# Performance work log

Measured on AMD Instinct MI355X. Metric: run time of the kernel, lower is better.

## Reference

```python
import math
import jax, jax.numpy as jnp
import numpy as np

LENGTHS = [1024, 768, 512, 1024, 256, 896, 640, 512]  # ragged seq lens, sum = 5632
NEG = -10000.0  # mask fill value used by the torch module


def setup_inputs() -> dict:
    key = jax.random.key(0)
    k1, k2 = jax.random.split(key)
    total = int(sum(LENGTHS))  # 5632 packed tokens
    H, HKV, D = 16, 4, 64      # GQA: 16 query heads, 4 kv heads
    q = jax.random.normal(k1, (total, H, D), dtype=jnp.float32)
    kv = jax.random.normal(k2, (total, 2, HKV, D), dtype=jnp.float32)
    cu_seqlens = jnp.asarray(np.concatenate([[0], np.cumsum(LENGTHS)]), dtype=jnp.int32)
    return {"q": q, "kv": kv, "cu_seqlens": cu_seqlens, "max_seqlen": 1024}


def _varlen_attention(q, kv, cu_seqlens, max_seqlen):
    # GQA repeat: '... hkv d -> ... (hkv g) d' == repeat each kv head g times
    g = q.shape[1] // kv.shape[2]
    kv = jnp.repeat(kv, g, axis=2)
    k, v = kv[:, 0], kv[:, 1]            # [total, H, D]

    starts = cu_seqlens[:-1]
    lens = cu_seqlens[1:] - starts       # [B]
    S = max_seqlen
    pos = jnp.arange(S)
    gather_idx = starts[:, None] + pos[None, :]          # [B, S]
    key_mask = pos[None, :] < lens[:, None]              # [B, S] True = valid
    gather_idx = jnp.where(key_mask, gather_idx, 0)

    m = key_mask[:, :, None, None]
    # pad ragged tokens into dense [B, S, H, D] buffers (zeros where invalid)
    qp = jnp.where(m, q[gather_idx], 0.0)
    kp = jnp.where(m, k[gather_idx], 0.0)
    vp = jnp.where(m, v[gather_idx], 0.0)

    scale = 1.0 / math.sqrt(q.shape[-1])
    scores = jnp.einsum('bthd,bshd->bhts', qp, kp * scale)   # [B, H, S, S]
    # key padding mask: 0 on valid keys, -10000 on padded keys
    scores = scores + jnp.where(key_mask, 0.0, NEG)[:, None, None, :]
    # causal mask: triu(-10000, 1)
    scores = scores + jnp.triu(jnp.full((S, S), NEG, dtype=scores.dtype), 1)

    attn = jax.nn.softmax(scores, axis=-1)
    out_padded = jnp.einsum('bhts,bshd->bthd', attn, vp)     # [B, S, H, D]

    # unpad back to packed [total, H, D]
    tok = jnp.arange(q.shape[0])
    b = jnp.searchsorted(cu_seqlens, tok, side='right') - 1  # batch id per token
    s = tok - starts[b]                                      # position within seq
    return out_padded[b, s]


def reference(q, kv, cu_seqlens, max_seqlen):
    return _varlen_attention(q, kv, cu_seqlens, max_seqlen)
```

## Files before the change

### kernel.cpp

```cpp
#include <hip/hip_runtime.h>


#define H    16
#define HKV  4
#define D    64
#define BM   16
#define BN   64
#define KSTR 72
#define NEGF (-1e30f)

using bf8 = __attribute__((ext_vector_type(8))) short;
using s4v = __attribute__((ext_vector_type(4))) short;
using f4v = __attribute__((ext_vector_type(4))) float;

__device__ inline short f2b(float x) {
    union { float f; unsigned u; } v; v.f = x;
    return (short)((v.u + 0x8000u) >> 16);
}

__global__ __launch_bounds__(256, 4)
void attn3(const float* __restrict__ q, const float* __restrict__ kv,
           const int* __restrict__ cu, float* __restrict__ out,
           int nb, int total)
{
    __shared__ __attribute__((aligned(16))) short Ks[BN * KSTR];
    __shared__ __attribute__((aligned(16))) short Vt[D * KSTR];
    __shared__ __attribute__((aligned(16))) short Ps[4][BM * KSTR];

    const int kvh = blockIdx.y;

    int bid = blockIdx.x, b = -1, start = 0, len = 0, q0 = 0, acc = 0;
    for (int i = 0; i < nb; ++i) {
        int s0 = cu[i], l = cu[i + 1] - s0, nt = (l + BM - 1) / BM;
        if (bid < acc + nt) { b = i; start = s0; len = l; q0 = (nt - 1 - (bid - acc)) * BM; break; }
        acc += nt;
    }
    if (b < 0) return;

    const int t = threadIdx.x, w = t >> 6, lane = t & 63;
    const int qd = lane >> 4, c = lane & 15;
    const int h = kvh * 4 + w;
    const int rows = min(BM, len - q0), kend = q0 + rows;
    const float SC = 0.125f * 1.44269504f;

    bf8 qf0, qf1;
    {
        int qr = min(c, rows - 1);
        const float* qp = q + (size_t)(start + q0 + qr) * (H * D) + h * D + qd * 8;
        float4 a0 = *(const float4*)qp;
        float4 a1 = *(const float4*)(qp + 4);
        float4 a2 = *(const float4*)(qp + 32);
        float4 a3 = *(const float4*)(qp + 36);
        qf0[0] = f2b(a0.x * SC); qf0[1] = f2b(a0.y * SC); qf0[2] = f2b(a0.z * SC); qf0[3] = f2b(a0.w * SC);
        qf0[4] = f2b(a1.x * SC); qf0[5] = f2b(a1.y * SC); qf0[6] = f2b(a1.z * SC); qf0[7] = f2b(a1.w * SC);
        qf1[0] = f2b(a2.x * SC); qf1[1] = f2b(a2.y * SC); qf1[2] = f2b(a2.z * SC); qf1[3] = f2b(a2.w * SC);
        qf1[4] = f2b(a3.x * SC); qf1[5] = f2b(a3.y * SC); qf1[6] = f2b(a3.z * SC); qf1[7] = f2b(a3.w * SC);
    }

    const int kd4 = t & 15, kr0 = t >> 4;
    const int vd  = t & 63, vg0 = t >> 6;

    float4 kreg[4];
    float  vreg[4][4];

    auto prefetch = [&](int kt0) {
        #pragma unroll
        for (int i = 0; i < 4; ++i) {
            int tok = min(start + kt0 + kr0 + 16 * i, total - 1);
            kreg[i] = *(const float4*)&kv[(size_t)tok * (2 * HKV * D) + kvh * D + kd4 * 4];
        }
        #pragma unroll
        for (int i = 0; i < 4; ++i) {
            int kg = vg0 + 4 * i;
            #pragma unroll
            for (int m = 0; m < 4; ++m) {
                int tok = min(start + kt0 + kg * 4 + m, total - 1);
                vreg[i][m] = kv[(size_t)tok * (2 * HKV * D) + (HKV + kvh) * D + vd];
            }
        }
    };

    float m_i = NEGF, l_i = 0.f;
    f4v o0 = {0,0,0,0}, o1 = {0,0,0,0}, o2 = {0,0,0,0}, o3 = {0,0,0,0};
    short* Psw = &Ps[w][0];

    prefetch(0);

    for (int kt0 = 0; kt0 < kend; kt0 += BN) {
        __syncthreads();
        #pragma unroll
        for (int i = 0; i < 4; ++i) {
            s4v p; p[0] = f2b(kreg[i].x); p[1] = f2b(kreg[i].y);
                   p[2] = f2b(kreg[i].z); p[3] = f2b(kreg[i].w);
            *(s4v*)&Ks[(kr0 + 16 * i) * KSTR + kd4 * 4] = p;
        }
        #pragma unroll
        for (int i = 0; i < 4; ++i) {
            int kg = vg0 + 4 * i;
            s4v p; p[0] = f2b(vreg[i][0]); p[1] = f2b(vreg[i][1]);
                   p[2] = f2b(vreg[i][2]); p[3] = f2b(vreg[i][3]);
            *(s4v*)&Vt[vd * KSTR + kg * 4] = p;
        }
        __syncthreads();

        if (kt0 + BN < kend) prefetch(kt0 + BN);

        f4v s0 = {0,0,0,0}, s1 = {0,0,0,0}, s2 = {0,0,0,0}, s3 = {0,0,0,0};
        {
            bf8 ka, kb;
            ka = *(const bf8*)&Ks[(c     ) * KSTR + qd * 8];
            kb = *(const bf8*)&Ks[(c     ) * KSTR + 32 + qd * 8];
            s0 = __builtin_amdgcn_mfma_f32_16x16x32_bf16(ka, qf0, s0, 0, 0, 0);
            s0 = __builtin_amdgcn_mfma_f32_16x16x32_bf16(kb, qf1, s0, 0, 0, 0);
            ka = *(const bf8*)&Ks[(16 + c) * KSTR + qd * 8];
            kb = *(const bf8*)&Ks[(16 + c) * KSTR + 32 + qd * 8];
            s1 = __builtin_amdgcn_mfma_f32_16x16x32_bf16(ka, qf0, s1, 0, 0, 0);
            s1 = __builtin_amdgcn_mfma_f32_16x16x32_bf16(kb, qf1, s1, 0, 0, 0);
            ka = *(const bf8*)&Ks[(32 + c) * KSTR + qd * 8];
            kb = *(const bf8*)&Ks[(32 + c) * KSTR + 32 + qd * 8];
            s2 = __builtin_amdgcn_mfma_f32_16x16x32_bf16(ka, qf0, s2, 0, 0, 0);
            s2 = __builtin_amdgcn_mfma_f32_16x16x32_bf16(kb, qf1, s2, 0, 0, 0);
            ka = *(const bf8*)&Ks[(48 + c) * KSTR + qd * 8];
            kb = *(const bf8*)&Ks[(48 + c) * KSTR + 32 + qd * 8];
            s3 = __builtin_amdgcn_mfma_f32_16x16x32_bf16(ka, qf0, s3, 0, 0, 0);
            s3 = __builtin_amdgcn_mfma_f32_16x16x32_bf16(kb, qf1, s3, 0, 0, 0);
        }

        const int limit = q0 + c - kt0;
        float sc[16];
        #pragma unroll
        for (int r = 0; r < 4; ++r) {
            sc[r]      = (      4 * qd + r <= limit) ? s0[r] : NEGF;
            sc[4 + r]  = (16 +  4 * qd + r <= limit) ? s1[r] : NEGF;
            sc[8 + r]  = (32 +  4 * qd + r <= limit) ? s2[r] : NEGF;
            sc[12 + r] = (48 +  4 * qd + r <= limit) ? s3[r] : NEGF;
        }
        float mt = sc[0];
        #pragma unroll
        for (int i = 1; i < 16; ++i) mt = fmaxf(mt, sc[i]);
        mt = fmaxf(mt, __shfl_xor(mt, 16, 64));
        mt = fmaxf(mt, __shfl_xor(mt, 32, 64));
        const float m_new = fmaxf(m_i, mt);
        const float alpha = exp2f(m_i - m_new);
        float ps = 0.f;
        #pragma unroll
        for (int i = 0; i < 16; ++i) { sc[i] = exp2f(sc[i] - m_new); ps += sc[i]; }
        ps += __shfl_xor(ps, 16, 64);
        ps += __shfl_xor(ps, 32, 64);
        l_i = l_i * alpha + ps;
        m_i = m_new;
        o0 *= alpha; o1 *= alpha; o2 *= alpha; o3 *= alpha;

        #pragma unroll
        for (int j = 0; j < 4; ++j) {
            s4v p; p[0] = f2b(sc[4 * j]);     p[1] = f2b(sc[4 * j + 1]);
                   p[2] = f2b(sc[4 * j + 2]); p[3] = f2b(sc[4 * j + 3]);
            *(s4v*)&Psw[c * KSTR + 16 * j + 4 * qd] = p;
        }
        bf8 p0 = *(const bf8*)&Psw[c * KSTR + qd * 8];
        bf8 p1 = *(const bf8*)&Psw[c * KSTR + 32 + qd * 8];

        o0 = __builtin_amdgcn_mfma_f32_16x16x32_bf16(*(const bf8*)&Vt[(c     ) * KSTR + qd * 8],      p0, o0, 0, 0, 0);
        o0 = __builtin_amdgcn_mfma_f32_16x16x32_bf16(*(const bf8*)&Vt[(c     ) * KSTR + 32 + qd * 8], p1, o0, 0, 0, 0);
        o1 = __builtin_amdgcn_mfma_f32_16x16x32_bf16(*(const bf8*)&Vt[(16 + c) * KSTR + qd * 8],      p0, o1, 0, 0, 0);
        o1 = __builtin_amdgcn_mfma_f32_16x16x32_bf16(*(const bf8*)&Vt[(16 + c) * KSTR + 32 + qd * 8], p1, o1, 0, 0, 0);
        o2 = __builtin_amdgcn_mfma_f32_16x16x32_bf16(*(const bf8*)&Vt[(32 + c) * KSTR + qd * 8],      p0, o2, 0, 0, 0);
        o2 = __builtin_amdgcn_mfma_f32_16x16x32_bf16(*(const bf8*)&Vt[(32 + c) * KSTR + 32 + qd * 8], p1, o2, 0, 0, 0);
        o3 = __builtin_amdgcn_mfma_f32_16x16x32_bf16(*(const bf8*)&Vt[(48 + c) * KSTR + qd * 8],      p0, o3, 0, 0, 0);
        o3 = __builtin_amdgcn_mfma_f32_16x16x32_bf16(*(const bf8*)&Vt[(48 + c) * KSTR + 32 + qd * 8], p1, o3, 0, 0, 0);
    }

    if (c < rows) {
        const float inv = 1.f / l_i;
        float* op = out + (size_t)(start + q0 + c) * (H * D) + h * D + 4 * qd;
        *(float4*)(op)      = make_float4(o0[0] * inv, o0[1] * inv, o0[2] * inv, o0[3] * inv);
        *(float4*)(op + 16) = make_float4(o1[0] * inv, o1[1] * inv, o1[2] * inv, o1[3] * inv);
        *(float4*)(op + 32) = make_float4(o2[0] * inv, o2[1] * inv, o2[2] * inv, o2[3] * inv);
        *(float4*)(op + 48) = make_float4(o3[0] * inv, o3[1] * inv, o3[2] * inv, o3[3] * inv);
    }
}

extern "C" void kernel_launch(void* const* d_in, const int* in_sizes, int n_in,
                              void* d_out, int out_size, void* d_ws, size_t ws_size,
                              hipStream_t stream) {
    const float* q  = (const float*)d_in[0];
    const float* kv = (const float*)d_in[1];
    const int*   cu = (const int*)d_in[2];
    float* out = (float*)d_out;

    const int total = in_sizes[0] / (H * D);
    const int nb    = in_sizes[2] - 1;
    const int tile_ub = total / BM + nb;

    dim3 grid(tile_ub, HKV);
    attn3<<<grid, 256, 0, stream>>>(q, kv, cu, out, nb, total);
}
```

Measured before the change: 129.6 us.

## Split KV loop across two warp groups with LDS merge of softmax partials

```diff
diff --git a/kernel.cpp b/kernel.cpp
--- a/kernel.cpp
+++ b/kernel.cpp
@@ -10,22 +10,27 @@
 #define NEGF (-1e30f)
 
 using bf8 = __attribute__((ext_vector_type(8))) short;
-using s4v = __attribute__((ext_vector_type(4))) short;
 using f4v = __attribute__((ext_vector_type(4))) float;
-
-__device__ inline short f2b(float x) {
-    union { float f; unsigned u; } v; v.f = x;
-    return (short)((v.u + 0x8000u) >> 16);
+typedef unsigned int u32;
+
+union bf8u { bf8 v; u32 w[4]; };
+
+__device__ inline u32 pk(float a, float b) {
+    union { float f; u32 u; } x, y; x.f = a; y.f = b;
+    return __builtin_amdgcn_perm(y.u + 0x8000u, x.u + 0x8000u, 0x07060302u);
 }
 
-__global__ __launch_bounds__(256, 4)
-void attn3(const float* __restrict__ q, const float* __restrict__ kv,
+#define MFMA(A, B, C) __builtin_amdgcn_mfma_f32_16x16x32_bf16(A, B, C, 0, 0, 0)
+
+__global__ __launch_bounds__(512, 4)
+void attn4(const float* __restrict__ q, const float* __restrict__ kv,
            const int* __restrict__ cu, float* __restrict__ out,
            int nb, int total)
 {
-    __shared__ __attribute__((aligned(16))) short Ks[BN * KSTR];
-    __shared__ __attribute__((aligned(16))) short Vt[D * KSTR];
-    __shared__ __attribute__((aligned(16))) short Ps[4][BM * KSTR];
+    __shared__ __attribute__((aligned(16))) short Ks[2][BN * KSTR];
+    __shared__ __attribute__((aligned(16))) short Vt[2][D * KSTR];
+    __shared__ __attribute__((aligned(16))) short Ps[8][BM * KSTR];
+    __shared__ float ML[4][BM][2];
 
     const int kvh = blockIdx.y;
 
@@ -38,12 +43,15 @@
     if (b < 0) return;
 
     const int t = threadIdx.x, w = t >> 6, lane = t & 63;
+    const int head = w & 3, g = w >> 2, u = t & 255;
     const int qd = lane >> 4, c = lane & 15;
-    const int h = kvh * 4 + w;
+    const int h = kvh * 4 + head;
     const int rows = min(BM, len - q0), kend = q0 + rows;
+    const int niter = (kend + BN - 1) >> 6;
+    const int trips = (niter + 1) >> 1;
     const float SC = 0.125f * 1.44269504f;
 
-    bf8 qf0, qf1;
+    bf8u qf0, qf1;
     {
         int qr = min(c, rows - 1);
         const float* qp = q + (size_t)(start + q0 + qr) * (H * D) + h * D + qd * 8;
@@ -51,90 +59,96 @@
         float4 a1 = *(const float4*)(qp + 4);
         float4 a2 = *(const float4*)(qp + 32);
         float4 a3 = *(const float4*)(qp + 36);
-        qf0[0] = f2b(a0.x * SC); qf0[1] = f2b(a0.y * SC); qf0[2] = f2b(a0.z * SC); qf0[3] = f2b(a0.w * SC);
-        qf0[4] = f2b(a1.x * SC); qf0[5] = f2b(a1.y * SC); qf0[6] = f2b(a1.z * SC); qf0[7] = f2b(a1.w * SC);
-        qf1[0] = f2b(a2.x * SC); qf1[1] = f2b(a2.y * SC); qf1[2] = f2b(a2.z * SC); qf1[3] = f2b(a2.w * SC);
-        qf1[4] = f2b(a3.x * SC); qf1[5] = f2b(a3.y * SC); qf1[6] = f2b(a3.z * SC); qf1[7] = f2b(a3.w * SC);
-    }
-
-    const int kd4 = t & 15, kr0 = t >> 4;
-    const int vd  = t & 63, vg0 = t >> 6;
-
-    float4 kreg[4];
-    float  vreg[4][4];
+        qf0.w[0] = pk(a0.x * SC, a0.y * SC); qf0.w[1] = pk(a0.z * SC, a0.w * SC);
+        qf0.w[2] = pk(a1.x * SC, a1.y * SC); qf0.w[3] = pk(a1.z * SC, a1.w * SC);
+        qf1.w[0] = pk(a2.x * SC, a2.y * SC); qf1.w[1] = pk(a2.z * SC, a2.w * SC);
+        qf1.w[2] = pk(a3.x * SC, a3.y * SC); qf1.w[3] = pk(a3.z * SC, a3.w * SC);
+    }
+
+    const int kd4 = u & 15, kr = u >> 4;
+    const int vkp = u & 15, vd4 = u >> 4;
+    const float* kbase = kv + kvh * D;
+    const float* vbase = kv + (HKV + kvh) * D;
+    float4 kreg[4], vreg[2][2];
 
     auto prefetch = [&](int kt0) {
         #pragma unroll
         for (int i = 0; i < 4; ++i) {
-            int tok = min(start + kt0 + kr0 + 16 * i, total - 1);
-            kreg[i] = *(const float4*)&kv[(size_t)tok * (2 * HKV * D) + kvh * D + kd4 * 4];
-        }
-        #pragma unroll
-        for (int i = 0; i < 4; ++i) {
-            int kg = vg0 + 4 * i;
-            #pragma unroll
-            for (int m = 0; m < 4; ++m) {
-                int tok = min(start + kt0 + kg * 4 + m, total - 1);
-                vreg[i][m] = kv[(size_t)tok * (2 * HKV * D) + (HKV + kvh) * D + vd];
-            }
+            int tok = min(start + kt0 + kr + 16 * i, total - 1);
+            kreg[i] = *(const float4*)(kbase + (size_t)tok * 512 + kd4 * 4);
+        }
+        #pragma unroll
+        for (int p = 0; p < 2; ++p) {
+            int k0 = start + kt0 + 2 * vkp + 32 * p;
+            int t0 = min(k0, total - 1), t1 = min(k0 + 1, total - 1);
+            vreg[p][0] = *(const float4*)(vbase + (size_t)t0 * 512 + vd4 * 4);
+            vreg[p][1] = *(const float4*)(vbase + (size_t)t1 * 512 + vd4 * 4);
         }
     };
 
     float m_i = NEGF, l_i = 0.f;
     f4v o0 = {0,0,0,0}, o1 = {0,0,0,0}, o2 = {0,0,0,0}, o3 = {0,0,0,0};
     short* Psw = &Ps[w][0];
-
-    prefetch(0);
-
-    for (int kt0 = 0; kt0 < kend; kt0 += BN) {
+    short* Kg  = &Ks[g][0];
+    short* Vg  = &Vt[g][0];
+
+    prefetch(g * BN);
+
+    for (int tp = 0; tp < trips; ++tp) {
+        const int it = 2 * tp + g, kt0 = it * BN;
+        const bool valid = it < niter;
         __syncthreads();
-        #pragma unroll
-        for (int i = 0; i < 4; ++i) {
-            s4v p; p[0] = f2b(kreg[i].x); p[1] = f2b(kreg[i].y);
-                   p[2] = f2b(kreg[i].z); p[3] = f2b(kreg[i].w);
-            *(s4v*)&Ks[(kr0 + 16 * i) * KSTR + kd4 * 4] = p;
-        }
-        #pragma unroll
-        for (int i = 0; i < 4; ++i) {
-            int kg = vg0 + 4 * i;
-            s4v p; p[0] = f2b(vreg[i][0]); p[1] = f2b(vreg[i][1]);
-                   p[2] = f2b(vreg[i][2]); p[3] = f2b(vreg[i][3]);
-            *(s4v*)&Vt[vd * KSTR + kg * 4] = p;
+        if (valid) {
+            #pragma unroll
+            for (int i = 0; i < 4; ++i) {
+                u32 lo = pk(kreg[i].x, kreg[i].y), hi = pk(kreg[i].z, kreg[i].w);
+                *(uint2*)&Kg[(kr + 16 * i) * KSTR + kd4 * 4] = make_uint2(lo, hi);
+            }
+            #pragma unroll
+            for (int p = 0; p < 2; ++p) {
+                const float* va = &vreg[p][0].x;
+                const float* vb = &vreg[p][1].x;
+                #pragma unroll
+                for (int j = 0; j < 4; ++j)
+                    *(u32*)&Vg[(4 * vd4 + j) * KSTR + 2 * vkp + 32 * p] = pk(va[j], vb[j]);
+            }
         }
         __syncthreads();
 
-        if (kt0 + BN < kend) prefetch(kt0 + BN);
+        if (2 * tp + 2 + g < niter) prefetch((2 * tp + 2 + g) * BN);
+        if (!valid) continue;
 
         f4v s0 = {0,0,0,0}, s1 = {0,0,0,0}, s2 = {0,0,0,0}, s3 = {0,0,0,0};
         {
             bf8 ka, kb;
-            ka = *(const bf8*)&Ks[(c     ) * KSTR + qd * 8];
-            kb = *(const bf8*)&Ks[(c     ) * KSTR + 32 + qd * 8];
-            s0 = __builtin_amdgcn_mfma_f32_16x16x32_bf16(ka, qf0, s0, 0, 0, 0);
-            s0 = __builtin_amdgcn_mfma_f32_16x16x32_bf16(kb, qf1, s0, 0, 0, 0);
-            ka = *(const bf8*)&Ks[(16 + c) * KSTR + qd * 8];
-            kb = *(const bf8*)&Ks[(16 + c) * KSTR + 32 + qd * 8];
-            s1 = __builtin_amdgcn_mfma_f32_16x16x32_bf16(ka, qf0, s1, 0, 0, 0);
-            s1 = __builtin_amdgcn_mfma_f32_16x16x32_bf16(kb, qf1, s1, 0, 0, 0);
-            ka = *(const bf8*)&Ks[(32 + c) * KSTR + qd * 8];
-            kb = *(const bf8*)&Ks[(32 + c) * KSTR + 32 + qd * 8];
-            s2 = __builtin_amdgcn_mfma_f32_16x16x32_bf16(ka, qf0, s2, 0, 0, 0);
-            s2 = __builtin_amdgcn_mfma_f32_16x16x32_bf16(kb, qf1, s2, 0, 0, 0);
-            ka = *(const bf8*)&Ks[(48 + c) * KSTR + qd * 8];
-            kb = *(const bf8*)&Ks[(48 + c) * KSTR + 32 + qd * 8];
-            s3 = __builtin_amdgcn_mfma_f32_16x16x32_bf16(ka, qf0, s3, 0, 0, 0);
-            s3 = __builtin_amdgcn_mfma_f32_16x16x32_bf16(kb, qf1, s3, 0, 0, 0);
-        }
-
-        const int limit = q0 + c - kt0;
+            ka = *(const bf8*)&Kg[(c     ) * KSTR + qd * 8];
+            kb = *(const bf8*)&Kg[(c     ) * KSTR + 32 + qd * 8];
+            s0 = MFMA(ka, qf0.v, s0); s0 = MFMA(kb, qf1.v, s0);
+            ka = *(const bf8*)&Kg[(16 + c) * KSTR + qd * 8];
+            kb = *(const bf8*)&Kg[(16 + c) * KSTR + 32 + qd * 8];
+            s1 = MFMA(ka, qf0.v, s1); s1 = MFMA(kb, qf1.v, s1);
+            ka = *(const bf8*)&Kg[(32 + c) * KSTR + qd * 8];
+            kb = *(const bf8*)&Kg[(32 + c) * KSTR + 32 + qd * 8];
+            s2 = MFMA(ka, qf0.v, s2); s2 = MFMA(kb, qf1.v, s2);
+            ka = *(const bf8*)&Kg[(48 + c) * KSTR + qd * 8];
+            kb = *(const bf8*)&Kg[(48 + c) * KSTR + 32 + qd * 8];
+            s3 = MFMA(ka, qf0.v, s3); s3 = MFMA(kb, qf1.v, s3);
+        }
+
         float sc[16];
         #pragma unroll
         for (int r = 0; r < 4; ++r) {
-            sc[r]      = (      4 * qd + r <= limit) ? s0[r] : NEGF;
-            sc[4 + r]  = (16 +  4 * qd + r <= limit) ? s1[r] : NEGF;
-            sc[8 + r]  = (32 +  4 * qd + r <= limit) ? s2[r] : NEGF;
-            sc[12 + r] = (48 +  4 * qd + r <= limit) ? s3[r] : NEGF;
-        }
+            sc[r] = s0[r]; sc[4 + r] = s1[r]; sc[8 + r] = s2[r]; sc[12 + r] = s3[r];
+        }
+        if (kt0 + 63 > q0) {
+            const int limit = q0 + c - kt0;
+            #pragma unroll
+            for (int j = 0; j < 4; ++j)
+                #pragma unroll
+                for (int r = 0; r < 4; ++r)
+                    if (16 * j + 4 * qd + r > limit) sc[4 * j + r] = NEGF;
+        }
+
         float mt = sc[0];
         #pragma unroll
         for (int i = 1; i < 16; ++i) mt = fmaxf(mt, sc[i]);
@@ -153,30 +167,49 @@
 
         #pragma unroll
         for (int j = 0; j < 4; ++j) {
-            s4v p; p[0] = f2b(sc[4 * j]);     p[1] = f2b(sc[4 * j + 1]);
-                   p[2] = f2b(sc[4 * j + 2]); p[3] = f2b(sc[4 * j + 3]);
-            *(s4v*)&Psw[c * KSTR + 16 * j + 4 * qd] = p;
+            u32 lo = pk(sc[4 * j], sc[4 * j + 1]), hi = pk(sc[4 * j + 2], sc[4 * j + 3]);
+            *(uint2*)&Psw[c * KSTR + 16 * j + 4 * qd] = make_uint2(lo, hi);
         }
         bf8 p0 = *(const bf8*)&Psw[c * KSTR + qd * 8];
         bf8 p1 = *(const bf8*)&Psw[c * KSTR + 32 + qd * 8];
 
-        o0 = __builtin_amdgcn_mfma_f32_16x16x32_bf16(*(const bf8*)&Vt[(c     ) * KSTR + qd * 8],      p0, o0, 0, 0, 0);
-        o0 = __builtin_amdgcn_mfma_f32_16x16x32_bf16(*(const bf8*)&Vt[(c     ) * KSTR + 32 + qd * 8], p1, o0, 0, 0, 0);
-        o1 = __builtin_amdgcn_mfma_f32_16x16x32_bf16(*(const bf8*)&Vt[(16 + c) * KSTR + qd * 8],      p0, o1, 0, 0, 0);
-        o1 = __builtin_amdgcn_mfma_f32_16x16x32_bf16(*(const bf8*)&Vt[(16 + c) * KSTR + 32 + qd * 8], p1, o1, 0, 0, 0);
-        o2 = __builtin_amdgcn_mfma_f32_16x16x32_bf16(*(const bf8*)&Vt[(32 + c) * KSTR + qd * 8],      p0, o2, 0, 0, 0);
-        o2 = __builtin_amdgcn_mfma_f32_16x16x32_bf16(*(const bf8*)&Vt[(32 + c) * KSTR + 32 + qd * 8], p1, o2, 0, 0, 0);
-        o3 = __builtin_amdgcn_mfma_f32_16x16x32_bf16(*(const bf8*)&Vt[(48 + c) * KSTR + qd * 8],      p0, o3, 0, 0, 0);
-        o3 = __builtin_amdgcn_mfma_f32_16x16x32_bf16(*(const bf8*)&Vt[(48 + c) * KSTR + 32 + qd * 8], p1, o3, 0, 0, 0);
-    }
-
-    if (c < rows) {
-        const float inv = 1.f / l_i;
+        o0 = MFMA(*(const bf8*)&Vg[(c     ) * KSTR + qd * 8],      p0, o0);
+        o0 = MFMA(*(const bf8*)&Vg[(c     ) * KSTR + 32 + qd * 8], p1, o0);
+        o1 = MFMA(*(const bf8*)&Vg[(16 + c) * KSTR + qd * 8],      p0, o1);
+        o1 = MFMA(*(const bf8*)&Vg[(16 + c) * KSTR + 32 + qd * 8], p1, o1);
+        o2 = MFMA(*(const bf8*)&Vg[(32 + c) * KSTR + qd * 8],      p0, o2);
+        o2 = MFMA(*(const bf8*)&Vg[(32 + c) * KSTR + 32 + qd * 8], p1, o2);
+        o3 = MFMA(*(const bf8*)&Vg[(48 + c) * KSTR + qd * 8],      p0, o3);
+        o3 = MFMA(*(const bf8*)&Vg[(48 + c) * KSTR + 32 + qd * 8], p1, o3);
+    }
+
+    float* CB = (float*)&Ks[0][0];
+    __syncthreads();
+    if (g == 1) {
+        float* cb = CB + (((head << 6) + lane) << 4);
+        *(f4v*)(cb)      = o0; *(f4v*)(cb + 4)  = o1;
+        *(f4v*)(cb + 8)  = o2; *(f4v*)(cb + 12) = o3;
+        if (qd == 0) { ML[head][c][0] = m_i; ML[head][c][1] = l_i; }
+    }
+    __syncthreads();
+    if (g == 0 && c < rows) {
+        const float* cb = CB + (((head << 6) + lane) << 4);
+        f4v r0 = *(const f4v*)(cb),     r1 = *(const f4v*)(cb + 4);
+        f4v r2 = *(const f4v*)(cb + 8), r3 = *(const f4v*)(cb + 12);
+        const float m2 = ML[head][c][0], l2 = ML[head][c][1];
+        const float M  = fmaxf(m_i, m2);
+        float a1 = exp2f(m_i - M), a2 = exp2f(m2 - M);
+        const float inv = 1.f / (l_i * a1 + l2 * a2);
+        a1 *= inv; a2 *= inv;
         float* op = out + (size_t)(start + q0 + c) * (H * D) + h * D + 4 * qd;
-        *(float4*)(op)      = make_float4(o0[0] * inv, o0[1] * inv, o0[2] * inv, o0[3] * inv);
-        *(float4*)(op + 16) = make_float4(o1[0] * inv, o1[1] * inv, o1[2] * inv, o1[3] * inv);
-        *(float4*)(op + 32) = make_float4(o2[0] * inv, o2[1] * inv, o2[2] * inv, o2[3] * inv);
-        *(float4*)(op + 48) = make_float4(o3[0] * inv, o3[1] * inv, o3[2] * inv, o3[3] * inv);
+        *(float4*)(op)      = make_float4(o0[0]*a1 + r0[0]*a2, o0[1]*a1 + r0[1]*a2,
+                                          o0[2]*a1 + r0[2]*a2, o0[3]*a1 + r0[3]*a2);
+        *(float4*)(op + 16) = make_float4(o1[0]*a1 + r1[0]*a2, o1[1]*a1 + r1[1]*a2,
+                                          o1[2]*a1 + r1[2]*a2, o1[3]*a1 + r1[3]*a2);
+        *(float4*)(op + 32) = make_float4(o2[0]*a1 + r2[0]*a2, o2[1]*a1 + r2[1]*a2,
+                                          o2[2]*a1 + r2[2]*a2, o2[3]*a1 + r2[3]*a2);
+        *(float4*)(op + 48) = make_float4(o3[0]*a1 + r3[0]*a2, o3[1]*a1 + r3[1]*a2,
+                                          o3[2]*a1 + r3[2]*a2, o3[3]*a1 + r3[3]*a2);
     }
 }
 
@@ -193,5 +226,5 @@
     const int tile_ub = total / BM + nb;
 
     dim3 grid(tile_ub, HKV);
-    attn3<<<grid, 256, 0, stream>>>(q, kv, cu, out, nb, total);
+    attn4<<<grid, 512, 0, stream>>>(q, kv, cu, out, nb, total);
 }
```

Measured after the change: 129.3 us. No clear change (-0.2%).
